# Optimization experiments

Measured on AMD Instinct MI355X. Metric: run time of the kernel, lower is better.

The kernel has to match this reference:

```python
import jax, jax.numpy as jnp
import numpy as np

B, C, N = 8, 256, 2048
H = max(1, C // 8)  # hidden = in_channels // 8 = 32


def setup_inputs() -> dict:
    key = jax.random.key(0)
    ks = jax.random.split(key, 7)
    s = 0.05
    return {
        "x": jax.random.normal(ks[0], (B, C, N), dtype=jnp.float32),
        "wq": jax.random.normal(ks[1], (H, C), dtype=jnp.float32) * s,
        "bq": jax.random.normal(ks[2], (H,), dtype=jnp.float32) * s,
        "wk": jax.random.normal(ks[3], (H, C), dtype=jnp.float32) * s,
        "bk": jax.random.normal(ks[4], (H,), dtype=jnp.float32) * s,
        "wv": jax.random.normal(ks[5], (C, C), dtype=jnp.float32) * s,
        "bv": jax.random.normal(ks[6], (C,), dtype=jnp.float32) * s,
    }


def reference(x, wq, bq, wk, bk, wv, bv):
    # 1x1 Conv1d == per-position linear: weight [out, in]
    q = jnp.einsum('bcn,hc->bnh', x, wq) + bq                  # [B, N, H] (already permuted)
    k = jnp.einsum('bcn,hc->bhn', x, wk) + bk[None, :, None]   # [B, H, N]
    v = jnp.einsum('bcn,dc->bdn', x, wv) + bv[None, :, None]   # [B, C, N]
    energy = jnp.einsum('bnh,bhm->bnm', q, k)                  # [B, N, N] (no scaling, as in source)
    weights = jax.nn.softmax(energy, axis=-1)                  # softmax over last dim
    # out = bmm(value, weights^T): out[b,c,i] = sum_j v[b,c,j] * weights[b,i,j]
    out = jnp.einsum('bcj,bij->bci', v, weights)               # [B, C, N]
    return out + x
```

## Files before the change

kernel.cpp:

```cpp
#include <hip/hip_runtime.h>
#include <hip/hip_bf16.h>
#include <cstdint>
#include <cstddef>

#define B_ 8
#define C_ 256
#define N_ 2048
#define H_ 32

typedef __bf16 bf8 __attribute__((ext_vector_type(8)));
typedef float f4 __attribute__((ext_vector_type(4)));
typedef float f16v __attribute__((ext_vector_type(16)));

__device__ inline void gload_lds16(const void* g, void* l) {
  __builtin_amdgcn_global_load_lds(
      (const __attribute__((address_space(1))) unsigned int*)g,
      (__attribute__((address_space(3))) unsigned int*)l, 16, 0, 0);
}

__global__ __launch_bounds__(256) void pack_kernel(
    const float* __restrict__ wq, const float* __restrict__ wk,
    const float* __restrict__ wv, const float* __restrict__ bq,
    const float* __restrict__ bk, const float* __restrict__ bv,
    __hip_bfloat16* __restrict__ wpk, float* __restrict__ bpk) {
  int r = blockIdx.x, c = threadIdx.x;
  float v;
  if (r < 256)      v = wv[r * 256 + c];
  else if (r < 288) v = wq[(r - 256) * 256 + c];
  else              v = wk[(r - 288) * 256 + c];
  wpk[r * 256 + c] = __float2bfloat16(v);
  if (c == 0) bpk[r] = (r < 256) ? bv[r] : (r < 288 ? bq[r - 256] : bk[r - 288]);
}

__global__ __launch_bounds__(256) void proj_kernel(
    const float* __restrict__ x, const __hip_bfloat16* __restrict__ wpk,
    const float* __restrict__ bpk, __hip_bfloat16* __restrict__ vbf,
    __hip_bfloat16* __restrict__ qkb) {
  __shared__ __attribute__((aligned(16))) __hip_bfloat16 As[2][320 * 32];
  int tid = threadIdx.x, wv = tid >> 6, lane = tid & 63;
  int b = blockIdx.y;
  int n0 = blockIdx.x * 32;
  int fcol = lane & 15, hi4 = lane >> 4;
  int grow = lane >> 2, gc = (lane & 3) * 8;
  const float* xb = x + (size_t)b * C_ * N_;

#pragma unroll
  for (int g = 0; g < 5; ++g)
    gload_lds16(wpk + (size_t)(wv * 80 + g * 16 + grow) * 256 + gc,
                &As[0][(wv * 80 + g * 16) * 32]);
  float xr[2][8];
#pragma unroll
  for (int j = 0; j < 2; ++j)
#pragma unroll
    for (int e = 0; e < 8; ++e)
      xr[j][e] = xb[(size_t)(hi4 * 8 + e) * N_ + n0 + j * 16 + fcol];

  f4 acc[5][2] = {};
  for (int t = 0; t < 8; ++t) {
    int buf = t & 1;
    __syncthreads();
    if (t < 7) {
      int k1 = (t + 1) * 32;
#pragma unroll
      for (int g = 0; g < 5; ++g)
        gload_lds16(wpk + (size_t)(wv * 80 + g * 16 + grow) * 256 + k1 + gc,
                    &As[buf ^ 1][(wv * 80 + g * 16) * 32]);
    }
    bf8 bfr[2];
#pragma unroll
    for (int j = 0; j < 2; ++j)
#pragma unroll
      for (int e = 0; e < 8; ++e) bfr[j][e] = (__bf16)xr[j][e];
    if (t < 7) {
      int k1 = (t + 1) * 32;
#pragma unroll
      for (int j = 0; j < 2; ++j)
#pragma unroll
        for (int e = 0; e < 8; ++e)
          xr[j][e] = xb[(size_t)(k1 + hi4 * 8 + e) * N_ + n0 + j * 16 + fcol];
    }
#pragma unroll
    for (int s = 0; s < 5; ++s) {
      bf8 af = *(const bf8*)&As[buf][(wv * 80 + s * 16 + fcol) * 32 + hi4 * 8];
      acc[s][0] = __builtin_amdgcn_mfma_f32_16x16x32_bf16(af, bfr[0], acc[s][0], 0, 0, 0);
      acc[s][1] = __builtin_amdgcn_mfma_f32_16x16x32_bf16(af, bfr[1], acc[s][1], 0, 0, 0);
    }
  }
  int rq = hi4 * 4;
#pragma unroll
  for (int s = 0; s < 5; ++s)
#pragma unroll
    for (int r = 0; r < 4; ++r) {
      int m = wv * 80 + s * 16 + rq + r;
      float bias = bpk[m];
#pragma unroll
      for (int j = 0; j < 2; ++j) {
        int n = n0 + j * 16 + fcol;
        float val = acc[s][j][r] + bias;
        if (m < 256)
          vbf[((size_t)b * C_ + m) * N_ + n] = __float2bfloat16(val);
        else
          qkb[((size_t)b * N_ + n) * 64 + (m - 256)] = __float2bfloat16(val);
      }
    }
}

#define FJT 64

__global__ __launch_bounds__(256, 2) void fused_attn(
    const __hip_bfloat16* __restrict__ qk,
    const __hip_bfloat16* __restrict__ vbf,
    const float* __restrict__ x, float* __restrict__ out) {
  __shared__ __attribute__((aligned(16))) __hip_bfloat16 vS[2][128 * FJT];
  __shared__ __attribute__((aligned(16))) __hip_bfloat16 pS[2][2][32 * 72];
  __shared__ float lSp[2][2][32];
  int tid = threadIdx.x;
  int wv = tid >> 6, lane = tid & 63;
  int iw = wv >> 1, cw = wv & 1;
  int blk = blockIdx.x;
  int b = blk & 7;
  int rest = blk >> 3;
  int c0 = (rest & 1) * 128;
  int i0 = (rest >> 1) * 64;
  int l31 = lane & 31, hi = lane >> 5;

  const __hip_bfloat16* qkB = qk + (size_t)b * N_ * 64;
  bf8 qf0 = *(const bf8*)&qkB[(size_t)(i0 + iw * 32 + l31) * 64 + hi * 8];
  bf8 qf1 = *(const bf8*)&qkB[(size_t)(i0 + iw * 32 + l31) * 64 + 16 + hi * 8];

  const __hip_bfloat16* vB = vbf + ((size_t)b * C_ + c0) * N_;
  int grow = lane >> 3;
  int gch = ((lane & 7) ^ (grow & 7)) * 8;
  int kjrow = cw * 32 + l31;

  bf8 kf0, kf1, kn0, kn1;
#pragma unroll
  for (int g = 0; g < 4; ++g)
    gload_lds16(vB + (size_t)(wv * 32 + g * 8 + grow) * N_ + gch,
                &vS[0][(wv * 32 + g * 8) * FJT]);
  kf0 = *(const bf8*)&qkB[(size_t)kjrow * 64 + 32 + hi * 8];
  kf1 = *(const bf8*)&qkB[(size_t)kjrow * 64 + 32 + 16 + hi * 8];

  f16v acc0 = {}, acc1 = {};
  float lp[16];
#pragma unroll
  for (int r = 0; r < 16; ++r) lp[r] = 0.f;

  for (int t = 0; t < N_ / FJT; ++t) {
    int buf = t & 1;
    f16v s = {};
    s = __builtin_amdgcn_mfma_f32_32x32x16_bf16(qf0, kf0, s, 0, 0, 0);
    s = __builtin_amdgcn_mfma_f32_32x32x16_bf16(qf1, kf1, s, 0, 0, 0);
    __hip_bfloat16* pW = &pS[buf][iw][0];
#pragma unroll
    for (int r = 0; r < 16; ++r) {
      float p = __expf(s[r]);
      lp[r] += p;
      int row = (r & 3) + 8 * (r >> 2) + 4 * hi;
      pW[row * 72 + cw * 32 + l31] = __float2bfloat16(p);
    }
    __syncthreads();
    if (t + 1 < N_ / FJT) {
      int j1 = (t + 1) * FJT;
#pragma unroll
      for (int g = 0; g < 4; ++g)
        gload_lds16(vB + (size_t)(wv * 32 + g * 8 + grow) * N_ + j1 + gch,
                    &vS[buf ^ 1][(wv * 32 + g * 8) * FJT]);
      kn0 = *(const bf8*)&qkB[(size_t)(j1 + kjrow) * 64 + 32 + hi * 8];
      kn1 = *(const bf8*)&qkB[(size_t)(j1 + kjrow) * 64 + 32 + 16 + hi * 8];
    }
    const __hip_bfloat16* pR = &pS[buf][iw][0];
    int r0 = cw * 64 + l31, r1 = r0 + 32;
    int sw = r0 & 7;
#pragma unroll
    for (int jc = 0; jc < 4; ++jc) {
      int ch = jc * 2 + hi;
      bf8 pf = *(const bf8*)&pR[l31 * 72 + jc * 16 + hi * 8];
      bf8 vf0 = *(const bf8*)&vS[buf][r0 * FJT + ((ch ^ sw) * 8)];
      bf8 vf1 = *(const bf8*)&vS[buf][r1 * FJT + ((ch ^ sw) * 8)];
      acc0 = __builtin_amdgcn_mfma_f32_32x32x16_bf16(vf0, pf, acc0, 0, 0, 0);
      acc1 = __builtin_amdgcn_mfma_f32_32x32x16_bf16(vf1, pf, acc1, 0, 0, 0);
    }
    if (t + 1 < N_ / FJT) { kf0 = kn0; kf1 = kn1; }
  }

#pragma unroll
  for (int r = 0; r < 16; ++r) {
    float v = lp[r];
    v += __shfl_xor(v, 1); v += __shfl_xor(v, 2); v += __shfl_xor(v, 4);
    v += __shfl_xor(v, 8); v += __shfl_xor(v, 16);
    lp[r] = v;
  }
  if (l31 == 0) {
#pragma unroll
    for (int r = 0; r < 16; ++r)
      lSp[iw][cw][(r & 3) + 8 * (r >> 2) + 4 * hi] = lp[r];
  }
  __syncthreads();
  float linv = 1.0f / (lSp[iw][0][l31] + lSp[iw][1][l31]);
  int i = i0 + iw * 32 + l31;
  const float* xr = x + (size_t)b * C_ * N_;
  float* op = out + (size_t)b * C_ * N_;
#pragma unroll
  for (int r = 0; r < 16; ++r) {
    int row = (r & 3) + 8 * (r >> 2) + 4 * hi;
    size_t o0 = (size_t)(c0 + cw * 64 + row) * N_ + i;
    op[o0] = acc0[r] * linv + xr[o0];
    size_t o1 = o0 + (size_t)32 * N_;
    op[o1] = acc1[r] * linv + xr[o1];
  }
}

extern "C" void kernel_launch(void* const* d_in, const int* in_sizes, int n_in,
                              void* d_out, int out_size, void* d_ws, size_t ws_size,
                              hipStream_t stream) {
  const float* x  = (const float*)d_in[0];
  const float* wq = (const float*)d_in[1];
  const float* bq = (const float*)d_in[2];
  const float* wk = (const float*)d_in[3];
  const float* bk = (const float*)d_in[4];
  const float* wv = (const float*)d_in[5];
  const float* bv = (const float*)d_in[6];
  float* out = (float*)d_out;

  char* ws = (char*)d_ws;
  __hip_bfloat16* qkb = (__hip_bfloat16*)ws;
  __hip_bfloat16* vbf = (__hip_bfloat16*)(ws + (2u << 20));
  __hip_bfloat16* wpk = (__hip_bfloat16*)(ws + (10u << 20));
  float*          bpk = (float*)(ws + (10u << 20) + (256u << 10));

  pack_kernel<<<dim3(320), 256, 0, stream>>>(wq, wk, wv, bq, bk, bv, wpk, bpk);
  proj_kernel<<<dim3(N_ / 32, B_), 256, 0, stream>>>(x, wpk, bpk, vbf, qkb);
  fused_attn<<<dim3(512), 256, 0, stream>>>(qkb, vbf, x, out);
}
```

Before: 134.9 us.

## Halve per-block tiles in projection and attention to double grid size

The projection kernel now covers 16 positions per block instead of 32, and the attention kernel covers 64 channels per block instead of 128. Both grids double, with occupancy raised to 4 blocks per CU for attention. The aim is to fill more of the GPU's compute units and hide latency better. In exchange, each attention block recomputes QK^T and exp for half as many channels, so score and softmax work doubles, and the weight tiles are re-read more often.

```diff
diff --git a/kernel.cpp b/kernel.cpp
--- a/kernel.cpp
+++ b/kernel.cpp
@@ -39,7 +39,7 @@
   __shared__ __attribute__((aligned(16))) __hip_bfloat16 As[2][320 * 32];
   int tid = threadIdx.x, wv = tid >> 6, lane = tid & 63;
   int b = blockIdx.y;
-  int n0 = blockIdx.x * 32;
+  int n0 = blockIdx.x * 16;
   int fcol = lane & 15, hi4 = lane >> 4;
   int grow = lane >> 2, gc = (lane & 3) * 8;
   const float* xb = x + (size_t)b * C_ * N_;
@@ -48,14 +48,12 @@
   for (int g = 0; g < 5; ++g)
     gload_lds16(wpk + (size_t)(wv * 80 + g * 16 + grow) * 256 + gc,
                 &As[0][(wv * 80 + g * 16) * 32]);
-  float xr[2][8];
-#pragma unroll
-  for (int j = 0; j < 2; ++j)
-#pragma unroll
-    for (int e = 0; e < 8; ++e)
-      xr[j][e] = xb[(size_t)(hi4 * 8 + e) * N_ + n0 + j * 16 + fcol];
-
-  f4 acc[5][2] = {};
+  float xr[8];
+#pragma unroll
+  for (int e = 0; e < 8; ++e)
+    xr[e] = xb[(size_t)(hi4 * 8 + e) * N_ + n0 + fcol];
+
+  f4 acc[5] = {};
   for (int t = 0; t < 8; ++t) {
     int buf = t & 1;
     __syncthreads();
@@ -66,52 +64,43 @@
         gload_lds16(wpk + (size_t)(wv * 80 + g * 16 + grow) * 256 + k1 + gc,
                     &As[buf ^ 1][(wv * 80 + g * 16) * 32]);
     }
-    bf8 bfr[2];
-#pragma unroll
-    for (int j = 0; j < 2; ++j)
-#pragma unroll
-      for (int e = 0; e < 8; ++e) bfr[j][e] = (__bf16)xr[j][e];
+    bf8 bfr;
+#pragma unroll
+    for (int e = 0; e < 8; ++e) bfr[e] = (__bf16)xr[e];
     if (t < 7) {
       int k1 = (t + 1) * 32;
 #pragma unroll
-      for (int j = 0; j < 2; ++j)
-#pragma unroll
-        for (int e = 0; e < 8; ++e)
-          xr[j][e] = xb[(size_t)(k1 + hi4 * 8 + e) * N_ + n0 + j * 16 + fcol];
+      for (int e = 0; e < 8; ++e)
+        xr[e] = xb[(size_t)(k1 + hi4 * 8 + e) * N_ + n0 + fcol];
     }
 #pragma unroll
     for (int s = 0; s < 5; ++s) {
       bf8 af = *(const bf8*)&As[buf][(wv * 80 + s * 16 + fcol) * 32 + hi4 * 8];
-      acc[s][0] = __builtin_amdgcn_mfma_f32_16x16x32_bf16(af, bfr[0], acc[s][0], 0, 0, 0);
-      acc[s][1] = __builtin_amdgcn_mfma_f32_16x16x32_bf16(af, bfr[1], acc[s][1], 0, 0, 0);
+      acc[s] = __builtin_amdgcn_mfma_f32_16x16x32_bf16(af, bfr, acc[s], 0, 0, 0);
     }
   }
   int rq = hi4 * 4;
+  int n = n0 + fcol;
 #pragma unroll
   for (int s = 0; s < 5; ++s)
 #pragma unroll
     for (int r = 0; r < 4; ++r) {
       int m = wv * 80 + s * 16 + rq + r;
-      float bias = bpk[m];
-#pragma unroll
-      for (int j = 0; j < 2; ++j) {
-        int n = n0 + j * 16 + fcol;
-        float val = acc[s][j][r] + bias;
-        if (m < 256)
-          vbf[((size_t)b * C_ + m) * N_ + n] = __float2bfloat16(val);
-        else
-          qkb[((size_t)b * N_ + n) * 64 + (m - 256)] = __float2bfloat16(val);
-      }
+      float val = acc[s][r] + bpk[m];
+      if (m < 256)
+        vbf[((size_t)b * C_ + m) * N_ + n] = __float2bfloat16(val);
+      else
+        qkb[((size_t)b * N_ + n) * 64 + (m - 256)] = __float2bfloat16(val);
     }
 }
 
 #define FJT 64
 
-__global__ __launch_bounds__(256, 2) void fused_attn(
+__global__ __launch_bounds__(256, 4) void fused_attn(
     const __hip_bfloat16* __restrict__ qk,
     const __hip_bfloat16* __restrict__ vbf,
     const float* __restrict__ x, float* __restrict__ out) {
-  __shared__ __attribute__((aligned(16))) __hip_bfloat16 vS[2][128 * FJT];
+  __shared__ __attribute__((aligned(16))) __hip_bfloat16 vS[2][64 * FJT];
   __shared__ __attribute__((aligned(16))) __hip_bfloat16 pS[2][2][32 * 72];
   __shared__ float lSp[2][2][32];
   int tid = threadIdx.x;
@@ -120,8 +109,8 @@
   int blk = blockIdx.x;
   int b = blk & 7;
   int rest = blk >> 3;
-  int c0 = (rest & 1) * 128;
-  int i0 = (rest >> 1) * 64;
+  int c0 = (rest & 3) * 64;
+  int i0 = (rest >> 2) * 64;
   int l31 = lane & 31, hi = lane >> 5;
 
   const __hip_bfloat16* qkB = qk + (size_t)b * N_ * 64;
@@ -135,13 +124,13 @@
 
   bf8 kf0, kf1, kn0, kn1;
 #pragma unroll
-  for (int g = 0; g < 4; ++g)
-    gload_lds16(vB + (size_t)(wv * 32 + g * 8 + grow) * N_ + gch,
-                &vS[0][(wv * 32 + g * 8) * FJT]);
+  for (int g = 0; g < 2; ++g)
+    gload_lds16(vB + (size_t)(wv * 16 + g * 8 + grow) * N_ + gch,
+                &vS[0][(wv * 16 + g * 8) * FJT]);
   kf0 = *(const bf8*)&qkB[(size_t)kjrow * 64 + 32 + hi * 8];
   kf1 = *(const bf8*)&qkB[(size_t)kjrow * 64 + 32 + 16 + hi * 8];
 
-  f16v acc0 = {}, acc1 = {};
+  f16v acc0 = {};
   float lp[16];
 #pragma unroll
   for (int r = 0; r < 16; ++r) lp[r] = 0.f;
@@ -163,23 +152,21 @@
     if (t + 1 < N_ / FJT) {
       int j1 = (t + 1) * FJT;
 #pragma unroll
-      for (int g = 0; g < 4; ++g)
-        gload_lds16(vB + (size_t)(wv * 32 + g * 8 + grow) * N_ + j1 + gch,
-                    &vS[buf ^ 1][(wv * 32 + g * 8) * FJT]);
+      for (int g = 0; g < 2; ++g)
+        gload_lds16(vB + (size_t)(wv * 16 + g * 8 + grow) * N_ + j1 + gch,
+                    &vS[buf ^ 1][(wv * 16 + g * 8) * FJT]);
       kn0 = *(const bf8*)&qkB[(size_t)(j1 + kjrow) * 64 + 32 + hi * 8];
       kn1 = *(const bf8*)&qkB[(size_t)(j1 + kjrow) * 64 + 32 + 16 + hi * 8];
     }
     const __hip_bfloat16* pR = &pS[buf][iw][0];
-    int r0 = cw * 64 + l31, r1 = r0 + 32;
+    int r0 = cw * 32 + l31;
     int sw = r0 & 7;
 #pragma unroll
     for (int jc = 0; jc < 4; ++jc) {
       int ch = jc * 2 + hi;
       bf8 pf = *(const bf8*)&pR[l31 * 72 + jc * 16 + hi * 8];
-      bf8 vf0 = *(const bf8*)&vS[buf][r0 * FJT + ((ch ^ sw) * 8)];
-      bf8 vf1 = *(const bf8*)&vS[buf][r1 * FJT + ((ch ^ sw) * 8)];
-      acc0 = __builtin_amdgcn_mfma_f32_32x32x16_bf16(vf0, pf, acc0, 0, 0, 0);
-      acc1 = __builtin_amdgcn_mfma_f32_32x32x16_bf16(vf1, pf, acc1, 0, 0, 0);
+      bf8 vf = *(const bf8*)&vS[buf][r0 * FJT + ((ch ^ sw) * 8)];
+      acc0 = __builtin_amdgcn_mfma_f32_32x32x16_bf16(vf, pf, acc0, 0, 0, 0);
     }
     if (t + 1 < N_ / FJT) { kf0 = kn0; kf1 = kn1; }
   }
@@ -204,10 +191,8 @@
 #pragma unroll
   for (int r = 0; r < 16; ++r) {
     int row = (r & 3) + 8 * (r >> 2) + 4 * hi;
-    size_t o0 = (size_t)(c0 + cw * 64 + row) * N_ + i;
+    size_t o0 = (size_t)(c0 + cw * 32 + row) * N_ + i;
     op[o0] = acc0[r] * linv + xr[o0];
-    size_t o1 = o0 + (size_t)32 * N_;
-    op[o1] = acc1[r] * linv + xr[o1];
   }
 }
 
@@ -230,6 +215,6 @@
   float*          bpk = (float*)(ws + (10u << 20) + (256u << 10));
 
   pack_kernel<<<dim3(320), 256, 0, stream>>>(wq, wk, wv, bq, bk, bv, wpk, bpk);
-  proj_kernel<<<dim3(N_ / 32, B_), 256, 0, stream>>>(x, wpk, bpk, vbf, qkb);
-  fused_attn<<<dim3(512), 256, 0, stream>>>(qkb, vbf, x, out);
-}
+  proj_kernel<<<dim3(N_ / 16, B_), 256, 0, stream>>>(x, wpk, bpk, vbf, qkb);
+  fused_attn<<<dim3(1024), 256, 0, stream>>>(qkb, vbf, x, out);
+}
```

Measured after the change: 152.4 us. 13.0% more time.

## Split attention key range across waves with register-resident P and LDS reduction

Applied to the files above, without the earlier changes.

The fused attention kernel now gives each wave a quarter of the key range for all 64 query rows and 128 channels. Softmax probabilities stay in registers, rearranged with lane shuffles, and V is read directly from global memory instead of being staged in shared memory with a barrier every tile. Per-wave partial outputs and row sums are combined through shared memory at the end. The projection kernel also double-buffers its x loads, transposes Q/K through shared memory for vectorized stores, and remaps its blocks to a 1D grid. Risks include high register pressure from eight 32x32 accumulators and uncoalesced global V loads.

```diff
diff --git a/kernel.cpp b/kernel.cpp
--- a/kernel.cpp
+++ b/kernel.cpp
@@ -6,7 +6,6 @@
 #define B_ 8
 #define C_ 256
 #define N_ 2048
-#define H_ 32
 
 typedef __bf16 bf8 __attribute__((ext_vector_type(8)));
 typedef float f4 __attribute__((ext_vector_type(4)));
@@ -16,6 +15,15 @@
   __builtin_amdgcn_global_load_lds(
       (const __attribute__((address_space(1))) unsigned int*)g,
       (__attribute__((address_space(3))) unsigned int*)l, 16, 0, 0);
+}
+
+__device__ inline uint32_t pk2(float a, float b) {
+  union { __bf16 h[2]; uint32_t u; } cv;
+  cv.h[0] = (__bf16)a; cv.h[1] = (__bf16)b; return cv.u;
+}
+__device__ inline bf8 mk8(uint32_t d0, uint32_t d1, uint32_t d2, uint32_t d3) {
+  union { uint32_t u[4]; bf8 v; } cv;
+  cv.u[0] = d0; cv.u[1] = d1; cv.u[2] = d2; cv.u[3] = d3; return cv.v;
 }
 
 __global__ __launch_bounds__(256) void pack_kernel(
@@ -37,9 +45,11 @@
     const float* __restrict__ bpk, __hip_bfloat16* __restrict__ vbf,
     __hip_bfloat16* __restrict__ qkb) {
   __shared__ __attribute__((aligned(16))) __hip_bfloat16 As[2][320 * 32];
+  __shared__ __attribute__((aligned(16))) __hip_bfloat16 qtr[32 * 72];
   int tid = threadIdx.x, wv = tid >> 6, lane = tid & 63;
-  int b = blockIdx.y;
-  int n0 = blockIdx.x * 32;
+  int blk = blockIdx.x;
+  int b = blk & 7;
+  int n0 = (blk >> 3) * 32;
   int fcol = lane & 15, hi4 = lane >> 4;
   int grow = lane >> 2, gc = (lane & 3) * 8;
   const float* xb = x + (size_t)b * C_ * N_;
@@ -48,20 +58,26 @@
   for (int g = 0; g < 5; ++g)
     gload_lds16(wpk + (size_t)(wv * 80 + g * 16 + grow) * 256 + gc,
                 &As[0][(wv * 80 + g * 16) * 32]);
-  float xr[2][8];
+  float xr[2][2][8];
 #pragma unroll
   for (int j = 0; j < 2; ++j)
 #pragma unroll
     for (int e = 0; e < 8; ++e)
-      xr[j][e] = xb[(size_t)(hi4 * 8 + e) * N_ + n0 + j * 16 + fcol];
+      xr[0][j][e] = xb[(size_t)(hi4 * 8 + e) * N_ + n0 + j * 16 + fcol];
 
   f4 acc[5][2] = {};
+#pragma unroll 1
   for (int t = 0; t < 8; ++t) {
     int buf = t & 1;
     __syncthreads();
     if (t < 7) {
       int k1 = (t + 1) * 32;
 #pragma unroll
+      for (int j = 0; j < 2; ++j)
+#pragma unroll
+        for (int e = 0; e < 8; ++e)
+          xr[buf ^ 1][j][e] = xb[(size_t)(k1 + hi4 * 8 + e) * N_ + n0 + j * 16 + fcol];
+#pragma unroll
       for (int g = 0; g < 5; ++g)
         gload_lds16(wpk + (size_t)(wv * 80 + g * 16 + grow) * 256 + k1 + gc,
                     &As[buf ^ 1][(wv * 80 + g * 16) * 32]);
@@ -70,15 +86,7 @@
 #pragma unroll
     for (int j = 0; j < 2; ++j)
 #pragma unroll
-      for (int e = 0; e < 8; ++e) bfr[j][e] = (__bf16)xr[j][e];
-    if (t < 7) {
-      int k1 = (t + 1) * 32;
-#pragma unroll
-      for (int j = 0; j < 2; ++j)
-#pragma unroll
-        for (int e = 0; e < 8; ++e)
-          xr[j][e] = xb[(size_t)(k1 + hi4 * 8 + e) * N_ + n0 + j * 16 + fcol];
-    }
+      for (int e = 0; e < 8; ++e) bfr[j][e] = (__bf16)xr[buf][j][e];
 #pragma unroll
     for (int s = 0; s < 5; ++s) {
       bf8 af = *(const bf8*)&As[buf][(wv * 80 + s * 16 + fcol) * 32 + hi4 * 8];
@@ -95,28 +103,31 @@
       float bias = bpk[m];
 #pragma unroll
       for (int j = 0; j < 2; ++j) {
-        int n = n0 + j * 16 + fcol;
+        int nl = j * 16 + fcol;
         float val = acc[s][j][r] + bias;
         if (m < 256)
-          vbf[((size_t)b * C_ + m) * N_ + n] = __float2bfloat16(val);
+          vbf[((size_t)b * C_ + m) * N_ + n0 + nl] = __float2bfloat16(val);
         else
-          qkb[((size_t)b * N_ + n) * 64 + (m - 256)] = __float2bfloat16(val);
+          qtr[nl * 72 + (m - 256)] = __float2bfloat16(val);
       }
     }
-}
-
-#define FJT 64
+  if (wv == 3) {
+#pragma unroll
+    for (int p = 0; p < 4; ++p) {
+      int nl = lane & 31, oct = (lane >> 5) + p * 2;
+      bf8 t8 = *(const bf8*)&qtr[nl * 72 + oct * 8];
+      *(bf8*)&qkb[((size_t)b * N_ + n0 + nl) * 64 + oct * 8] = t8;
+    }
+  }
+}
 
 __global__ __launch_bounds__(256, 2) void fused_attn(
     const __hip_bfloat16* __restrict__ qk,
     const __hip_bfloat16* __restrict__ vbf,
     const float* __restrict__ x, float* __restrict__ out) {
-  __shared__ __attribute__((aligned(16))) __hip_bfloat16 vS[2][128 * FJT];
-  __shared__ __attribute__((aligned(16))) __hip_bfloat16 pS[2][2][32 * 72];
-  __shared__ float lSp[2][2][32];
-  int tid = threadIdx.x;
-  int wv = tid >> 6, lane = tid & 63;
-  int iw = wv >> 1, cw = wv & 1;
+  __shared__ float obuf[4 * 128 * 32];
+  __shared__ float lbuf[4][2][32];
+  int tid = threadIdx.x, wv = tid >> 6, lane = tid & 63;
   int blk = blockIdx.x;
   int b = blk & 7;
   int rest = blk >> 3;
@@ -125,89 +136,130 @@
   int l31 = lane & 31, hi = lane >> 5;
 
   const __hip_bfloat16* qkB = qk + (size_t)b * N_ * 64;
-  bf8 qf0 = *(const bf8*)&qkB[(size_t)(i0 + iw * 32 + l31) * 64 + hi * 8];
-  bf8 qf1 = *(const bf8*)&qkB[(size_t)(i0 + iw * 32 + l31) * 64 + 16 + hi * 8];
-
   const __hip_bfloat16* vB = vbf + ((size_t)b * C_ + c0) * N_;
-  int grow = lane >> 3;
-  int gch = ((lane & 7) ^ (grow & 7)) * 8;
-  int kjrow = cw * 32 + l31;
-
-  bf8 kf0, kf1, kn0, kn1;
-#pragma unroll
-  for (int g = 0; g < 4; ++g)
-    gload_lds16(vB + (size_t)(wv * 32 + g * 8 + grow) * N_ + gch,
-                &vS[0][(wv * 32 + g * 8) * FJT]);
-  kf0 = *(const bf8*)&qkB[(size_t)kjrow * 64 + 32 + hi * 8];
-  kf1 = *(const bf8*)&qkB[(size_t)kjrow * 64 + 32 + 16 + hi * 8];
-
-  f16v acc0 = {}, acc1 = {};
-  float lp[16];
-#pragma unroll
-  for (int r = 0; r < 16; ++r) lp[r] = 0.f;
-
-  for (int t = 0; t < N_ / FJT; ++t) {
-    int buf = t & 1;
-    f16v s = {};
-    s = __builtin_amdgcn_mfma_f32_32x32x16_bf16(qf0, kf0, s, 0, 0, 0);
-    s = __builtin_amdgcn_mfma_f32_32x32x16_bf16(qf1, kf1, s, 0, 0, 0);
-    __hip_bfloat16* pW = &pS[buf][iw][0];
+
+  bf8 qf[2][2];
+#pragma unroll
+  for (int s = 0; s < 2; ++s)
+#pragma unroll
+    for (int f = 0; f < 2; ++f)
+      qf[s][f] = *(const bf8*)&qkB[(size_t)(i0 + s * 32 + l31) * 64 + f * 16 + hi * 8];
+
+  int jg0 = wv * 512;
+  bf8 kf[2], kn[2];
+#pragma unroll
+  for (int f = 0; f < 2; ++f)
+    kf[f] = *(const bf8*)&qkB[(size_t)(jg0 + l31) * 64 + 32 + f * 16 + hi * 8];
+
+  f16v acc0[4] = {}, acc1[4] = {};
+  float lp0 = 0.f, lp1 = 0.f;
+
+#pragma unroll 1
+  for (int t = 0; t < 16; ++t) {
+    int jg = jg0 + t * 32;
+    if (t < 15) {
+#pragma unroll
+      for (int f = 0; f < 2; ++f)
+        kn[f] = *(const bf8*)&qkB[(size_t)(jg + 32 + l31) * 64 + 32 + f * 16 + hi * 8];
+    }
+    bf8 vf[4][2];
+#pragma unroll
+    for (int mt = 0; mt < 2; ++mt)
+#pragma unroll
+      for (int f = 0; f < 2; ++f)
+        vf[mt][f] = *(const bf8*)&vB[(size_t)(mt * 32 + l31) * N_ + jg + f * 16 + hi * 8];
+    f16v s0 = {}, s1 = {};
+    s0 = __builtin_amdgcn_mfma_f32_32x32x16_bf16(kf[0], qf[0][0], s0, 0, 0, 0);
+    s0 = __builtin_amdgcn_mfma_f32_32x32x16_bf16(kf[1], qf[0][1], s0, 0, 0, 0);
+    s1 = __builtin_amdgcn_mfma_f32_32x32x16_bf16(kf[0], qf[1][0], s1, 0, 0, 0);
+    s1 = __builtin_amdgcn_mfma_f32_32x32x16_bf16(kf[1], qf[1][1], s1, 0, 0, 0);
+    uint32_t pk[8], sw[8];
+#pragma unroll
+    for (int u = 0; u < 8; ++u) {
+      float e0 = __expf(s0[2 * u]), e1 = __expf(s0[2 * u + 1]);
+      lp0 += e0 + e1;
+      pk[u] = pk2(e0, e1);
+    }
+#pragma unroll
+    for (int u = 0; u < 8; ++u) sw[u] = (uint32_t)__shfl_xor((int)pk[u], 32);
+    bf8 pf00 = mk8(hi ? sw[2] : pk[0], hi ? sw[3] : pk[1],
+                   hi ? pk[2] : sw[0], hi ? pk[3] : sw[1]);
+    bf8 pf01 = mk8(hi ? sw[6] : pk[4], hi ? sw[7] : pk[5],
+                   hi ? pk[6] : sw[4], hi ? pk[7] : sw[5]);
+#pragma unroll
+    for (int mt = 2; mt < 4; ++mt)
+#pragma unroll
+      for (int f = 0; f < 2; ++f)
+        vf[mt][f] = *(const bf8*)&vB[(size_t)(mt * 32 + l31) * N_ + jg + f * 16 + hi * 8];
+#pragma unroll
+    for (int u = 0; u < 8; ++u) {
+      float e0 = __expf(s1[2 * u]), e1 = __expf(s1[2 * u + 1]);
+      lp1 += e0 + e1;
+      pk[u] = pk2(e0, e1);
+    }
+#pragma unroll
+    for (int u = 0; u < 8; ++u) sw[u] = (uint32_t)__shfl_xor((int)pk[u], 32);
+    bf8 pf10 = mk8(hi ? sw[2] : pk[0], hi ? sw[3] : pk[1],
+                   hi ? pk[2] : sw[0], hi ? pk[3] : sw[1]);
+    bf8 pf11 = mk8(hi ? sw[6] : pk[4], hi ? sw[7] : pk[5],
+                   hi ? pk[6] : sw[4], hi ? pk[7] : sw[5]);
+#pragma unroll
+    for (int mt = 0; mt < 4; ++mt) {
+      acc0[mt] = __builtin_amdgcn_mfma_f32_32x32x16_bf16(vf[mt][0], pf00, acc0[mt], 0, 0, 0);
+      acc0[mt] = __builtin_amdgcn_mfma_f32_32x32x16_bf16(vf[mt][1], pf01, acc0[mt], 0, 0, 0);
+      acc1[mt] = __builtin_amdgcn_mfma_f32_32x32x16_bf16(vf[mt][0], pf10, acc1[mt], 0, 0, 0);
+      acc1[mt] = __builtin_amdgcn_mfma_f32_32x32x16_bf16(vf[mt][1], pf11, acc1[mt], 0, 0, 0);
+    }
+    kf[0] = kn[0]; kf[1] = kn[1];
+  }
+
+  lp0 += __shfl_xor(lp0, 32);
+  lp1 += __shfl_xor(lp1, 32);
+  if (hi == 0) { lbuf[wv][0][l31] = lp0; lbuf[wv][1][l31] = lp1; }
+
+  const float* xB = x + (size_t)b * C_ * N_;
+  float* oB = out + (size_t)b * C_ * N_;
+
+#pragma unroll
+  for (int mt = 0; mt < 4; ++mt)
 #pragma unroll
     for (int r = 0; r < 16; ++r) {
-      float p = __expf(s[r]);
-      lp[r] += p;
-      int row = (r & 3) + 8 * (r >> 2) + 4 * hi;
-      pW[row * 72 + cw * 32 + l31] = __float2bfloat16(p);
-    }
-    __syncthreads();
-    if (t + 1 < N_ / FJT) {
-      int j1 = (t + 1) * FJT;
-#pragma unroll
-      for (int g = 0; g < 4; ++g)
-        gload_lds16(vB + (size_t)(wv * 32 + g * 8 + grow) * N_ + j1 + gch,
-                    &vS[buf ^ 1][(wv * 32 + g * 8) * FJT]);
-      kn0 = *(const bf8*)&qkB[(size_t)(j1 + kjrow) * 64 + 32 + hi * 8];
-      kn1 = *(const bf8*)&qkB[(size_t)(j1 + kjrow) * 64 + 32 + 16 + hi * 8];
-    }
-    const __hip_bfloat16* pR = &pS[buf][iw][0];
-    int r0 = cw * 64 + l31, r1 = r0 + 32;
-    int sw = r0 & 7;
-#pragma unroll
-    for (int jc = 0; jc < 4; ++jc) {
-      int ch = jc * 2 + hi;
-      bf8 pf = *(const bf8*)&pR[l31 * 72 + jc * 16 + hi * 8];
-      bf8 vf0 = *(const bf8*)&vS[buf][r0 * FJT + ((ch ^ sw) * 8)];
-      bf8 vf1 = *(const bf8*)&vS[buf][r1 * FJT + ((ch ^ sw) * 8)];
-      acc0 = __builtin_amdgcn_mfma_f32_32x32x16_bf16(vf0, pf, acc0, 0, 0, 0);
-      acc1 = __builtin_amdgcn_mfma_f32_32x32x16_bf16(vf1, pf, acc1, 0, 0, 0);
-    }
-    if (t + 1 < N_ / FJT) { kf0 = kn0; kf1 = kn1; }
-  }
-
-#pragma unroll
-  for (int r = 0; r < 16; ++r) {
-    float v = lp[r];
-    v += __shfl_xor(v, 1); v += __shfl_xor(v, 2); v += __shfl_xor(v, 4);
-    v += __shfl_xor(v, 8); v += __shfl_xor(v, 16);
-    lp[r] = v;
-  }
-  if (l31 == 0) {
-#pragma unroll
-    for (int r = 0; r < 16; ++r)
-      lSp[iw][cw][(r & 3) + 8 * (r >> 2) + 4 * hi] = lp[r];
-  }
+      int row = mt * 32 + (r & 3) + 8 * (r >> 2) + 4 * hi;
+      obuf[(wv * 128 + row) * 32 + l31] = acc0[mt][r];
+    }
   __syncthreads();
-  float linv = 1.0f / (lSp[iw][0][l31] + lSp[iw][1][l31]);
-  int i = i0 + iw * 32 + l31;
-  const float* xr = x + (size_t)b * C_ * N_;
-  float* op = out + (size_t)b * C_ * N_;
-#pragma unroll
-  for (int r = 0; r < 16; ++r) {
-    int row = (r & 3) + 8 * (r >> 2) + 4 * hi;
-    size_t o0 = (size_t)(c0 + cw * 64 + row) * N_ + i;
-    op[o0] = acc0[r] * linv + xr[o0];
-    size_t o1 = o0 + (size_t)32 * N_;
-    op[o1] = acc1[r] * linv + xr[o1];
+  float linv0 = 1.f / (lbuf[0][0][l31] + lbuf[1][0][l31] + lbuf[2][0][l31] + lbuf[3][0][l31]);
+  float linv1 = 1.f / (lbuf[0][1][l31] + lbuf[1][1][l31] + lbuf[2][1][l31] + lbuf[3][1][l31]);
+  {
+    int ii = i0 + l31;
+#pragma unroll
+    for (int rr = 0; rr < 16; ++rr) {
+      int crow = wv * 32 + hi * 16 + rr;
+      float sum = obuf[crow * 32 + l31] + obuf[(128 + crow) * 32 + l31] +
+                  obuf[(256 + crow) * 32 + l31] + obuf[(384 + crow) * 32 + l31];
+      size_t off = (size_t)(c0 + crow) * N_ + ii;
+      oB[off] = sum * linv0 + xB[off];
+    }
+  }
+  __syncthreads();
+#pragma unroll
+  for (int mt = 0; mt < 4; ++mt)
+#pragma unroll
+    for (int r = 0; r < 16; ++r) {
+      int row = mt * 32 + (r & 3) + 8 * (r >> 2) + 4 * hi;
+      obuf[(wv * 128 + row) * 32 + l31] = acc1[mt][r];
+    }
+  __syncthreads();
+  {
+    int ii = i0 + 32 + l31;
+#pragma unroll
+    for (int rr = 0; rr < 16; ++rr) {
+      int crow = wv * 32 + hi * 16 + rr;
+      float sum = obuf[crow * 32 + l31] + obuf[(128 + crow) * 32 + l31] +
+                  obuf[(256 + crow) * 32 + l31] + obuf[(384 + crow) * 32 + l31];
+      size_t off = (size_t)(c0 + crow) * N_ + ii;
+      oB[off] = sum * linv1 + xB[off];
+    }
   }
 }
 
@@ -230,6 +282,6 @@
   float*          bpk = (float*)(ws + (10u << 20) + (256u << 10));
 
   pack_kernel<<<dim3(320), 256, 0, stream>>>(wq, wk, wv, bq, bk, bv, wpk, bpk);
-  proj_kernel<<<dim3(N_ / 32, B_), 256, 0, stream>>>(x, wpk, bpk, vbf, qkb);
+  proj_kernel<<<dim3(512), 256, 0, stream>>>(x, wpk, bpk, vbf, qkb);
   fused_attn<<<dim3(512), 256, 0, stream>>>(qkb, vbf, x, out);
 }
```

After: 144.9 us. +7.4%, slower.
